# Kernel optimization log

Measured on AMD Instinct MI355X. Metric: run time of the kernel, lower is better.

Reference implementation:

```python
import jax, jax.numpy as jnp
import numpy as np

D_MODEL = 1024
D_K = 1024
D_V = 1024


def setup_inputs() -> dict:
    key = jax.random.key(0)
    kx, kq, kk, kv = jax.random.split(key, 4)
    B, T = 4, 2048
    x = jax.random.normal(kx, (B, T, D_MODEL), dtype=jnp.float32)
    # nn.Linear(d_model, d_k, bias=False) weight has shape (d_k, d_model); y = x @ W.T
    s = 1.0 / np.sqrt(D_MODEL)
    Wq = jax.random.uniform(kq, (D_K, D_MODEL), jnp.float32, -s, s)
    Wk = jax.random.uniform(kk, (D_K, D_MODEL), jnp.float32, -s, s)
    Wv = jax.random.uniform(kv, (D_V, D_MODEL), jnp.float32, -s, s)
    return {"x": x, "Wq": Wq, "Wk": Wk, "Wv": Wv}


def reference(x, Wq, Wk, Wv):
    # x: [B, T, D]; W*: [d_out, D]
    Q = jnp.einsum('btd,kd->btk', x, Wq)  # [B, T, d_k]
    K = jnp.einsum('btd,kd->btk', x, Wk)  # [B, T, d_k]
    V = jnp.einsum('btd,vd->btv', x, Wv)  # [B, T, d_v]
    scores = jnp.einsum('btk,bsk->bts', Q, K) / jnp.sqrt(jnp.float32(D_K))
    attn = jax.nn.softmax(scores, axis=-1)
    out = jnp.einsum('bts,bsv->btv', attn, V)  # [B, T, d_v]
    return out
```

## Files before the change

### kernel.cpp

```cpp
#include <hip/hip_runtime.h>
#include <hip/hip_bf16.h>
#include <stdint.h>

#define TT     2048
#define DMODEL 1024
#define NBATCH 4

typedef __bf16 bf16x8 __attribute__((ext_vector_type(8)));
typedef __bf16 bf16x4 __attribute__((ext_vector_type(4)));
typedef float  f32x4  __attribute__((ext_vector_type(4)));

#define GPTR(p) ((const __attribute__((address_space(1))) void*)(p))
#define LPTR(p) ((__attribute__((address_space(3))) void*)(p))

__global__ __launch_bounds__(256) void cvt_f32_bf16(const float* __restrict__ in,
                                                    __bf16* __restrict__ out, int n4)
{
    int i = blockIdx.x * 256 + threadIdx.x;
    if (i < n4) {
        float4 v = ((const float4*)in)[i];
        bf16x4 o;
        o[0] = (__bf16)v.x; o[1] = (__bf16)v.y; o[2] = (__bf16)v.z; o[3] = (__bf16)v.w;
        ((bf16x4*)out)[i] = o;
    }
}

template <typename OutT, int BN, int WRN>
__global__ __launch_bounds__(512, 2) void gemm256(
    const __bf16* __restrict__ A, const __bf16* __restrict__ B,
    OutT* __restrict__ C, int N, int Kd,
    long sA, long sB, long sC, float scale)
{
    constexpr int WCN  = 8 / WRN;
    constexpr int WM   = 256 / WRN;
    constexpr int WN   = BN / WCN;
    constexpr int IW   = WM / 16;
    constexpr int IH   = IW / 2;
    constexpr int JW   = WN / 16;
    constexpr int JH   = JW / 2;
    constexpr int QB   = BN / 64;
    constexpr int BSTR = BN * 128;

    __shared__ __align__(16) char lds[65536 + 2 * BSTR];

    const int z = blockIdx.z;
    A += (size_t)z * (size_t)sA;
    B += (size_t)z * (size_t)sB;
    C += (size_t)z * (size_t)sC;

    const int tid  = threadIdx.x;
    const int lane = tid & 63;
    const int wid  = tid >> 6;
    const int wr   = wid / WCN;
    const int wc   = wid % WCN;
    const int kg   = lane >> 4;
    const int rl   = lane & 15;

    const int m0 = blockIdx.x * 256;
    const int n0 = blockIdx.y * BN;

    const int swzX   = (rl & 7) << 4;
    const int lo0    = ((0 << 6) | (kg << 4)) ^ swzX;
    const int lo1    = ((1 << 6) | (kg << 4)) ^ swzX;
    const int baseA  = wr * (WM * 128) + rl * 128;
    const int baseBr = wc * (WN * 128) + rl * 128;

    const int srow = tid >> 3;
    const int scol = (((tid & 7) * 16) ^ ((srow & 7) << 4)) >> 1;
    const __bf16* pA[4];
    const __bf16* pB[QB];
#pragma unroll
    for (int q = 0; q < 4; q++)  pA[q] = A + (size_t)(m0 + q * 64 + srow) * Kd + scol;
#pragma unroll
    for (int q = 0; q < QB; q++) pB[q] = B + (size_t)(n0 + q * 64 + srow) * Kd + scol;
    const int dstw = wid * 1024;

#define STAGE_A(buf) do { _Pragma("unroll")                                         \
    for (int q = 0; q < 4; q++) {                                                   \
        __builtin_amdgcn_global_load_lds(GPTR(pA[q]),                               \
            LPTR(lds + (buf) * 32768 + q * 8192 + dstw), 16, 0, 0);                 \
        pA[q] += 64;                                                                \
    } } while (0)

#define STAGE_B(buf) do { _Pragma("unroll")                                         \
    for (int q = 0; q < QB; q++) {                                                  \
        __builtin_amdgcn_global_load_lds(GPTR(pB[q]),                               \
            LPTR(lds + 65536 + (buf) * BSTR + q * 8192 + dstw), 16, 0, 0);          \
        pB[q] += 64;                                                                \
    } } while (0)

#define LDA(buf, mh) do { _Pragma("unroll")                                         \
    for (int i2 = 0; i2 < IH; i2++) {                                               \
        af[i2 * 2 + 0] = *(const bf16x8*)(lds + (buf) * 32768 + baseA + ((mh) * IH + i2) * 2048 + lo0); \
        af[i2 * 2 + 1] = *(const bf16x8*)(lds + (buf) * 32768 + baseA + ((mh) * IH + i2) * 2048 + lo1); \
    } } while (0)

#define LDB(buf, nh) do { _Pragma("unroll")                                         \
    for (int j2 = 0; j2 < JH; j2++) {                                               \
        bfr[((nh) * JH + j2) * 2 + 0] = *(const bf16x8*)(lds + 65536 + (buf) * BSTR + baseBr + ((nh) * JH + j2) * 2048 + lo0); \
        bfr[((nh) * JH + j2) * 2 + 1] = *(const bf16x8*)(lds + 65536 + (buf) * BSTR + baseBr + ((nh) * JH + j2) * 2048 + lo1); \
    } } while (0)

#define MMA(mh, nh) do { _Pragma("unroll")                                          \
    for (int i2 = 0; i2 < IH; i2++) { _Pragma("unroll")                             \
        for (int j2 = 0; j2 < JH; j2++) {                                           \
            const int f_ = (nh) * JH + j2;                                          \
            const int a_ = (mh) * IH + i2;                                          \
            acc[a_][f_] = __builtin_amdgcn_mfma_f32_16x16x32_bf16(                  \
                af[i2 * 2 + 0], bfr[f_ * 2 + 0], acc[a_][f_], 0, 0, 0);             \
            acc[a_][f_] = __builtin_amdgcn_mfma_f32_16x16x32_bf16(                  \
                af[i2 * 2 + 1], bfr[f_ * 2 + 1], acc[a_][f_], 0, 0, 0);             \
    } } } while (0)

#define BAR   asm volatile("s_barrier" ::: "memory")
#define VMC4  asm volatile("s_waitcnt vmcnt(4)" ::: "memory")
#define VMC0  asm volatile("s_waitcnt vmcnt(0)" ::: "memory")
#define PRIO1 __builtin_amdgcn_s_setprio(1)
#define PRIO0 __builtin_amdgcn_s_setprio(0)
#define SB0   __builtin_amdgcn_sched_barrier(0)

    f32x4 acc[IW][JW] = {};
    bf16x8 af[IH * 2], bfr[JW * 2];

    STAGE_A(0); STAGE_B(0); STAGE_A(1);
    VMC4; BAR;

    const int NT2 = Kd >> 7;
    for (int i = 0; i < NT2; ++i) {
        const bool nl = (i + 1 < NT2);
        STAGE_B(1);
        LDA(0, 0); LDB(0, 0);
        SB0; BAR; SB0; PRIO1; MMA(0, 0); PRIO0; SB0; BAR;
        LDB(0, 1);
        SB0; BAR; SB0; PRIO1; MMA(0, 1); PRIO0; SB0; BAR;
        LDA(0, 1);
        SB0; BAR; SB0; PRIO1; MMA(1, 0); PRIO0; SB0; BAR;
        if (nl) STAGE_A(0);
        SB0; PRIO1; MMA(1, 1); PRIO0; SB0;
        if (nl) { VMC4; } else { VMC0; }
        BAR;
        if (nl) STAGE_B(0);
        LDA(1, 0); LDB(1, 0);
        SB0; BAR; SB0; PRIO1; MMA(0, 0); PRIO0; SB0; BAR;
        LDB(1, 1);
        SB0; BAR; SB0; PRIO1; MMA(0, 1); PRIO0; SB0; BAR;
        LDA(1, 1);
        SB0; BAR; SB0; PRIO1; MMA(1, 0); PRIO0; SB0; BAR;
        if (nl) STAGE_A(1);
        SB0; PRIO1; MMA(1, 1); PRIO0; SB0;
        if (nl) { VMC4; BAR; }
    }

    const int rb = m0 + wr * WM + kg * 4;
    const int cb = n0 + wc * WN + rl;
#pragma unroll
    for (int i = 0; i < IW; i++)
#pragma unroll
        for (int j = 0; j < JW; j++)
#pragma unroll
            for (int r = 0; r < 4; r++)
                C[(size_t)(rb + i * 16 + r) * N + (cb + j * 16)] = (OutT)(acc[i][j][r] * scale);

#undef STAGE_A
#undef STAGE_B
#undef LDA
#undef LDB
#undef MMA
#undef BAR
#undef VMC4
#undef VMC0
#undef PRIO1
#undef PRIO0
#undef SB0
}

__global__ __launch_bounds__(256) void softmax_rows(__bf16* __restrict__ S)
{
    __shared__ float wred[4];
    const int row  = blockIdx.x;
    __bf16* p      = S + (size_t)row * TT;
    const int tid  = threadIdx.x;
    const int lane = tid & 63;
    const int wv   = tid >> 6;

    bf16x8 v = *(const bf16x8*)(p + tid * 8);
    float f[8];
    float m = -1e30f;
#pragma unroll
    for (int j = 0; j < 8; j++) { f[j] = (float)v[j]; m = fmaxf(m, f[j]); }
#pragma unroll
    for (int off = 32; off; off >>= 1) m = fmaxf(m, __shfl_xor(m, off, 64));
    if (lane == 0) wred[wv] = m;
    __syncthreads();
    m = fmaxf(fmaxf(wred[0], wred[1]), fmaxf(wred[2], wred[3]));
    __syncthreads();

    float s = 0.f;
#pragma unroll
    for (int j = 0; j < 8; j++) { f[j] = __expf(f[j] - m); s += f[j]; }
#pragma unroll
    for (int off = 32; off; off >>= 1) s += __shfl_xor(s, off, 64);
    if (lane == 0) wred[wv] = s;
    __syncthreads();
    s = wred[0] + wred[1] + wred[2] + wred[3];
    const float inv = 1.0f / s;

    bf16x8 o;
#pragma unroll
    for (int j = 0; j < 8; j++) o[j] = (__bf16)(f[j] * inv);
    *(bf16x8*)(p + tid * 8) = o;
}

extern "C" void kernel_launch(void* const* d_in, const int* in_sizes, int n_in,
                              void* d_out, int out_size, void* d_ws, size_t ws_size,
                              hipStream_t stream)
{
    const float* x  = (const float*)d_in[0];
    const float* Wq = (const float*)d_in[1];
    const float* Wk = (const float*)d_in[2];
    const float* Wv = (const float*)d_in[3];
    float* out = (float*)d_out;

    const size_t MT = (size_t)NBATCH * TT;
    __bf16* xb  = (__bf16*)d_ws;
    __bf16* wqb = xb  + MT * DMODEL;
    __bf16* wkb = wqb + (size_t)DMODEL * DMODEL;
    __bf16* wvb = wkb + (size_t)DMODEL * DMODEL;
    __bf16* Qb  = wvb + (size_t)DMODEL * DMODEL;
    __bf16* Kb  = Qb  + MT * DMODEL;
    __bf16* Vt  = Kb  + MT * DMODEL;
    __bf16* S   = Vt  + MT * DMODEL;

    cvt_f32_bf16<<<dim3((int)(MT * DMODEL / 4 / 256)), 256, 0, stream>>>(x, xb, (int)(MT * DMODEL / 4));
    cvt_f32_bf16<<<dim3(DMODEL * DMODEL / 4 / 256), 256, 0, stream>>>(Wq, wqb, DMODEL * DMODEL / 4);
    cvt_f32_bf16<<<dim3(DMODEL * DMODEL / 4 / 256), 256, 0, stream>>>(Wk, wkb, DMODEL * DMODEL / 4);
    cvt_f32_bf16<<<dim3(DMODEL * DMODEL / 4 / 256), 256, 0, stream>>>(Wv, wvb, DMODEL * DMODEL / 4);

    gemm256<__bf16, 256, 2><<<dim3(32, 4, 2), 512, 0, stream>>>(
        xb, wqb, Qb, DMODEL, DMODEL,
        0, (long)DMODEL * DMODEL, (long)MT * DMODEL, 1.0f);

    gemm256<__bf16, 128, 4><<<dim3(4, 16, NBATCH), 512, 0, stream>>>(
        wvb, xb, Vt, TT, DMODEL,
        0, (long)TT * DMODEL, (long)DMODEL * TT, 1.0f);

    gemm256<__bf16, 256, 2><<<dim3(8, 8, NBATCH), 512, 0, stream>>>(
        Qb, Kb, S, TT, DMODEL,
        (long)TT * DMODEL, (long)TT * DMODEL, (long)TT * TT, 0.03125f);

    softmax_rows<<<dim3(NBATCH * TT), 256, 0, stream>>>(S);

    gemm256<float, 128, 4><<<dim3(8, 8, NBATCH), 512, 0, stream>>>(
        S, Vt, out, DMODEL, TT,
        (long)TT * TT, (long)DMODEL * TT, (long)TT * DMODEL, 1.0f);
}
```

Baseline: 159.9 us.

## Remap GEMM blocks across XCDs and deepen B-tile prefetch in pipeline

```diff
diff --git a/kernel.cpp b/kernel.cpp
--- a/kernel.cpp
+++ b/kernel.cpp
@@ -25,7 +25,7 @@
     }
 }
 
-template <typename OutT, int BN, int WRN>
+template <typename OutT, int BN, int WRN, bool YMAJOR>
 __global__ __launch_bounds__(512, 2) void gemm256(
     const __bf16* __restrict__ A, const __bf16* __restrict__ B,
     OutT* __restrict__ C, int N, int Kd,
@@ -43,10 +43,17 @@
 
     __shared__ __align__(16) char lds[65536 + 2 * BSTR];
 
-    const int z = blockIdx.z;
-    A += (size_t)z * (size_t)sA;
-    B += (size_t)z * (size_t)sB;
-    C += (size_t)z * (size_t)sC;
+    const int nx = gridDim.x, ny = gridDim.y;
+    const int fid = blockIdx.x + nx * (blockIdx.y + ny * blockIdx.z);
+    const int chunk = (nx * ny * gridDim.z) >> 3;
+    const int g = (fid & 7) * chunk + (fid >> 3);
+    int bx, by, bz;
+    if (YMAJOR) { by = g % ny; int r = g / ny; bx = r % nx; bz = r / nx; }
+    else        { bx = g % nx; int r = g / nx; by = r % ny; bz = r / ny; }
+
+    A += (size_t)bz * (size_t)sA;
+    B += (size_t)bz * (size_t)sB;
+    C += (size_t)bz * (size_t)sC;
 
     const int tid  = threadIdx.x;
     const int lane = tid & 63;
@@ -56,8 +63,8 @@
     const int kg   = lane >> 4;
     const int rl   = lane & 15;
 
-    const int m0 = blockIdx.x * 256;
-    const int n0 = blockIdx.y * BN;
+    const int m0 = bx * 256;
+    const int n0 = by * BN;
 
     const int swzX   = (rl & 7) << 4;
     const int lo0    = ((0 << 6) | (kg << 4)) ^ swzX;
@@ -113,7 +120,8 @@
     } } } while (0)
 
 #define BAR   asm volatile("s_barrier" ::: "memory")
-#define VMC4  asm volatile("s_waitcnt vmcnt(4)" ::: "memory")
+#define VMCS  do { if constexpr (QB == 4) asm volatile("s_waitcnt vmcnt(8)" ::: "memory"); \
+                   else                   asm volatile("s_waitcnt vmcnt(6)" ::: "memory"); } while (0)
 #define VMC0  asm volatile("s_waitcnt vmcnt(0)" ::: "memory")
 #define PRIO1 __builtin_amdgcn_s_setprio(1)
 #define PRIO0 __builtin_amdgcn_s_setprio(0)
@@ -122,33 +130,33 @@
     f32x4 acc[IW][JW] = {};
     bf16x8 af[IH * 2], bfr[JW * 2];
 
-    STAGE_A(0); STAGE_B(0); STAGE_A(1);
-    VMC4; BAR;
+    STAGE_A(0); STAGE_B(0); STAGE_B(1); STAGE_A(1);
+    VMCS; BAR;
 
     const int NT2 = Kd >> 7;
     for (int i = 0; i < NT2; ++i) {
         const bool nl = (i + 1 < NT2);
-        STAGE_B(1);
         LDA(0, 0); LDB(0, 0);
         SB0; BAR; SB0; PRIO1; MMA(0, 0); PRIO0; SB0; BAR;
         LDB(0, 1);
         SB0; BAR; SB0; PRIO1; MMA(0, 1); PRIO0; SB0; BAR;
+        if (nl) STAGE_B(0);
         LDA(0, 1);
         SB0; BAR; SB0; PRIO1; MMA(1, 0); PRIO0; SB0; BAR;
         if (nl) STAGE_A(0);
         SB0; PRIO1; MMA(1, 1); PRIO0; SB0;
-        if (nl) { VMC4; } else { VMC0; }
+        if (nl) { VMCS; } else { VMC0; }
         BAR;
-        if (nl) STAGE_B(0);
         LDA(1, 0); LDB(1, 0);
         SB0; BAR; SB0; PRIO1; MMA(0, 0); PRIO0; SB0; BAR;
         LDB(1, 1);
         SB0; BAR; SB0; PRIO1; MMA(0, 1); PRIO0; SB0; BAR;
+        if (nl) STAGE_B(1);
         LDA(1, 1);
         SB0; BAR; SB0; PRIO1; MMA(1, 0); PRIO0; SB0; BAR;
         if (nl) STAGE_A(1);
         SB0; PRIO1; MMA(1, 1); PRIO0; SB0;
-        if (nl) { VMC4; BAR; }
+        if (nl) { VMCS; BAR; }
     }
 
     const int rb = m0 + wr * WM + kg * 4;
@@ -167,7 +175,7 @@
 #undef LDB
 #undef MMA
 #undef BAR
-#undef VMC4
+#undef VMCS
 #undef VMC0
 #undef PRIO1
 #undef PRIO0
@@ -236,21 +244,21 @@
     cvt_f32_bf16<<<dim3(DMODEL * DMODEL / 4 / 256), 256, 0, stream>>>(Wk, wkb, DMODEL * DMODEL / 4);
     cvt_f32_bf16<<<dim3(DMODEL * DMODEL / 4 / 256), 256, 0, stream>>>(Wv, wvb, DMODEL * DMODEL / 4);
 
-    gemm256<__bf16, 256, 2><<<dim3(32, 4, 2), 512, 0, stream>>>(
+    gemm256<__bf16, 256, 2, true><<<dim3(32, 4, 2), 512, 0, stream>>>(
         xb, wqb, Qb, DMODEL, DMODEL,
         0, (long)DMODEL * DMODEL, (long)MT * DMODEL, 1.0f);
 
-    gemm256<__bf16, 128, 4><<<dim3(4, 16, NBATCH), 512, 0, stream>>>(
+    gemm256<__bf16, 128, 4, false><<<dim3(4, 16, NBATCH), 512, 0, stream>>>(
         wvb, xb, Vt, TT, DMODEL,
         0, (long)TT * DMODEL, (long)DMODEL * TT, 1.0f);
 
-    gemm256<__bf16, 256, 2><<<dim3(8, 8, NBATCH), 512, 0, stream>>>(
+    gemm256<__bf16, 256, 2, false><<<dim3(8, 8, NBATCH), 512, 0, stream>>>(
         Qb, Kb, S, TT, DMODEL,
         (long)TT * DMODEL, (long)TT * DMODEL, (long)TT * TT, 0.03125f);
 
     softmax_rows<<<dim3(NBATCH * TT), 256, 0, stream>>>(S);
 
-    gemm256<float, 128, 4><<<dim3(8, 8, NBATCH), 512, 0, stream>>>(
+    gemm256<float, 128, 4, true><<<dim3(8, 8, NBATCH), 512, 0, stream>>>(
         S, Vt, out, DMODEL, TT,
         (long)TT * TT, (long)DMODEL * TT, (long)TT * DMODEL, 1.0f);
 }
```

Result: no change. 157.4 us (-1.5%).
